# Kernel optimization log

Hardware: AMD Instinct MI355X
Metric: run time of the kernel (lower is better)

Reference implementation:

```python
import jax, jax.numpy as jnp
import numpy as np
import math

B, S, DM, H = 2, 2048, 1024, 16
DH = DM // H  # 64


def setup_inputs() -> dict:
    key = jax.random.key(0)
    ks = jax.random.split(key, 12)
    s = 1.0 / math.sqrt(DM)
    inp = {
        "key": jax.random.normal(ks[0], (B, S, DM), jnp.float32),
        "value": jax.random.normal(ks[1], (B, S, DM), jnp.float32),
        "query": jax.random.normal(ks[2], (B, S, DM), jnp.float32),
        # causal mask: True = masked out (matches masked_fill semantics)
        "mask": jnp.broadcast_to(~jnp.tril(jnp.ones((S, S), bool)), (B, S, S)),
        "Wk": jax.random.normal(ks[3], (DM, DM), jnp.float32) * s,
        "bk": jnp.zeros((DM,), jnp.float32),
        "Wv": jax.random.normal(ks[4], (DM, DM), jnp.float32) * s,
        "bv": jnp.zeros((DM,), jnp.float32),
        "Wq": jax.random.normal(ks[5], (DM, DM), jnp.float32) * s,
        "bq": jnp.zeros((DM,), jnp.float32),
        "Wo": jax.random.normal(ks[6], (DM, DM), jnp.float32) * s,
        "bo": jnp.zeros((DM,), jnp.float32),
    }
    return inp


def _split_heads(x):
    # [B, S, H*DH] -> [B, H, S, DH]
    b, s, _ = x.shape
    return x.reshape(b, s, H, DH).transpose(0, 2, 1, 3)


def reference(key, value, query, mask, Wk, bk, Wv, bv, Wq, bq, Wo, bo):
    key_up = _split_heads(key @ Wk.T + bk)      # [B,H,S,DH]
    value_up = _split_heads(value @ Wv.T + bv)  # [B,H,S,DH]
    query_up = _split_heads(query @ Wq.T + bq) / math.sqrt(DH)
    scores = jnp.einsum("bhqd,bhkd->bhqk", query_up, key_up)  # [B,H,S,S]
    scores = jnp.where(mask[:, None, :, :], jnp.float32(-1e18), scores)
    attn = jax.nn.softmax(scores, axis=-1)
    # dropout is identity in eval mode
    context = jnp.einsum("bhqk,bhkd->bhqd", attn, value_up)
    context = context.transpose(0, 2, 1, 3).reshape(key.shape[0], -1, H * DH)
    output = context @ Wo.T + bo                # [B,S,DM]
    top_attn = attn[:, 0, :, :]                 # [B,S,S]
    return output, top_attn
```

## Files before the change

kernel.cpp:

```cpp
#include <hip/hip_runtime.h>
#include <hip/hip_bf16.h>
#include <math.h>

#define B_ 2
#define S_ 2048
#define DM_ 1024
#define H_ 16
#define DH_ 64

using short8 = __attribute__((ext_vector_type(8))) short;
using f32x4  = __attribute__((ext_vector_type(4))) float;

typedef const __attribute__((address_space(1))) void* gas_cvp;
typedef __attribute__((address_space(3))) void* las_vp;

struct CvtJobs {
    const float* in[7];
    ushort* out[7];
};

__device__ __forceinline__ ushort f2bu(float x) {
    __hip_bfloat16 h = __float2bfloat16(x);
    return *(ushort*)&h;
}

__global__ __launch_bounds__(256) void cvt_bf16(CvtJobs jobs) {
    const int bid = blockIdx.x;
    int j, blk;
    if (bid < 6144) { j = bid >> 11; blk = bid & 2047; }
    else { const int r = bid - 6144; j = 3 + (r >> 9); blk = r & 511; }
    const int idx = (blk * 256 + threadIdx.x) * 8;
    const float* in = jobs.in[j];
    float4 a = *(const float4*)&in[idx];
    float4 b = *(const float4*)&in[idx + 4];
    ushort u[8];
    u[0] = f2bu(a.x); u[1] = f2bu(a.y); u[2] = f2bu(a.z); u[3] = f2bu(a.w);
    u[4] = f2bu(b.x); u[5] = f2bu(b.y); u[6] = f2bu(b.z); u[7] = f2bu(b.w);
    *(int4*)&jobs.out[j][idx] = *(int4*)u;
}

#define GEMM_STAGE(buf, k0v)                                                   \
    {                                                                          \
        _Pragma("unroll")                                                      \
        for (int i = 0; i < 2; i++) {                                          \
            const int s   = i * 256 + tid;                                     \
            const int c   = s >> 7;                                            \
            const int row = s & 127;                                           \
            __builtin_amdgcn_global_load_lds(                                  \
                (gas_cvp)(Ag + (size_t)(i0 + row) * 1024 + (k0v) + c * 8),     \
                (las_vp)&AsB[buf][0][(i * 256 + w * 64) * 8], 16, 0, 0);       \
            __builtin_amdgcn_global_load_lds(                                  \
                (gas_cvp)(Wg + (size_t)(j0 + row) * 1024 + (k0v) + c * 8),     \
                (las_vp)&AsB[buf][1][(i * 256 + w * 64) * 8], 16, 0, 0);       \
        }                                                                      \
    }

#define GEMM_KLOOP()                                                           \
    {                                                                          \
        int bufc = 0;                                                          \
        GEMM_STAGE(0, 0);                                                      \
        GEMM_STAGE(1, 32);                                                     \
        for (int k0 = 0; k0 < 1024; k0 += 32) {                                \
            if (k0 + 32 < 1024)                                                \
                asm volatile("s_waitcnt vmcnt(4)" ::: "memory");               \
            else                                                               \
                asm volatile("s_waitcnt vmcnt(0)" ::: "memory");               \
            __builtin_amdgcn_s_barrier();                                      \
            if (k0 + 64 < 1024) {                                              \
                const int nb = (bufc + 2 >= 3) ? bufc - 1 : bufc + 2;          \
                GEMM_STAGE(nb, k0 + 64);                                       \
            }                                                                  \
            short8 af[4], bf[4];                                               \
            _Pragma("unroll")                                                  \
            for (int m = 0; m < 4; m++)                                        \
                af[m] = *(const short8*)&AsB[bufc][0][((g << 7) + wm * 64 + m * 16 + lr) * 8]; \
            _Pragma("unroll")                                                  \
            for (int n = 0; n < 4; n++)                                        \
                bf[n] = *(const short8*)&AsB[bufc][1][((g << 7) + wn * 64 + n * 16 + lr) * 8]; \
            _Pragma("unroll")                                                  \
            for (int m = 0; m < 4; m++)                                        \
                _Pragma("unroll")                                              \
                for (int n = 0; n < 4; n++)                                    \
                    acc[m][n] = __builtin_amdgcn_mfma_f32_16x16x32_bf16(       \
                        af[m], bf[n], acc[m][n], 0, 0, 0);                     \
            bufc = (bufc + 1 == 3) ? 0 : bufc + 1;                             \
        }                                                                      \
    }

struct ProjJobs {
    const ushort* A[3];
    const ushort* W[3];
    const float* bias[3];
    ushort* C[3];
    float scale[3];
};

__global__ __launch_bounds__(256) void gemm_proj3(ProjJobs jobs)
{
    __shared__ ushort AsB[3][2][4096];

    const int o   = blockIdx.x;
    const int swz = (o & 7) * 96 + (o >> 3);
    const int z   = swz >> 8;
    const int rem = swz & 255;
    const int by  = rem >> 3;
    const int bx  = rem & 7;

    const ushort* Ag = jobs.A[z];
    const ushort* Wg = jobs.W[z];
    const float* bias = jobs.bias[z];
    ushort* C = jobs.C[z];
    const float scale = jobs.scale[z];

    const int tid  = threadIdx.x;
    const int w    = tid >> 6;
    const int lane = tid & 63;
    const int g    = lane >> 4;
    const int lr   = lane & 15;
    const int wm   = w >> 1;
    const int wn   = w & 1;
    const int i0   = by * 128;
    const int j0   = bx * 128;

    f32x4 acc[4][4];
    #pragma unroll
    for (int m = 0; m < 4; m++)
        #pragma unroll
        for (int n = 0; n < 4; n++)
            #pragma unroll
            for (int jj = 0; jj < 4; jj++) acc[m][n][jj] = 0.f;

    GEMM_KLOOP();

    const int colbase = j0 + wn * 64;
    const int rowbase = i0 + wm * 64;
    #pragma unroll
    for (int n = 0; n < 4; n++) {
        const int col = colbase + n * 16 + lr;
        const float bb = bias[col];
        const int hh = col >> 6;
        const int d = col & 63;
        #pragma unroll
        for (int m = 0; m < 4; m++) {
            const int rb = rowbase + m * 16 + g * 4;
            #pragma unroll
            for (int jj = 0; jj < 4; jj++) {
                const float v = (acc[m][n][jj] + bb) * scale;
                const int i = rb + jj;
                const int b = i >> 11;
                const int srow = i & 2047;
                C[(((size_t)b * H_ + hh) * S_ + srow) * DH_ + d] = f2bu(v);
            }
        }
    }
}

__global__ __launch_bounds__(256) void flash_mfma(
    const ushort* __restrict__ Qb, const ushort* __restrict__ Kb,
    const ushort* __restrict__ Vb, __hip_bfloat16* __restrict__ ctx,
    float* __restrict__ m0, float* __restrict__ l0)
{
    const int bid = blockIdx.x;
    const int xcd = bid & 7;
    const int t   = bid >> 3;
    const int P   = (t >> 4) * 8 + xcd;
    const int p   = t & 15;
    const int h   = P & 15;
    const int b   = P >> 4;

    const int qtA = p, qtB = 31 - p;
    const size_t hoff = ((size_t)b * H_ + h) * S_ * DH_;
    const ushort* Qh = Qb + hoff;
    const ushort* Kh = Kb + hoff;
    const ushort* Vh = Vb + hoff;

    __shared__ ushort Ks[64][72];
    __shared__ ushort Vt[64][72];
    __shared__ ushort Ps[4][16][72];

    const int tid  = threadIdx.x;
    const int w    = tid >> 6;
    const int lane = tid & 63;
    const int g    = lane >> 4;
    const int lr   = lane & 15;
    const int q0A  = qtA * 64 + w * 16;
    const int q0B  = qtB * 64 + w * 16;

    short8 qfA0, qfA1, qfB0, qfB1;
    {
        const ushort* qa = Qh + (size_t)(q0A + lr) * DH_ + g * 8;
        qfA0 = *(const short8*)(qa);
        qfA1 = *(const short8*)(qa + 32);
        const ushort* qb = Qh + (size_t)(q0B + lr) * DH_ + g * 8;
        qfB0 = *(const short8*)(qb);
        qfB1 = *(const short8*)(qb + 32);
    }

    f32x4 oA[4], oB[4];
    #pragma unroll
    for (int nc = 0; nc < 4; nc++) {
        oA[nc][0]=0.f; oA[nc][1]=0.f; oA[nc][2]=0.f; oA[nc][3]=0.f;
        oB[nc][0]=0.f; oB[nc][1]=0.f; oB[nc][2]=0.f; oB[nc][3]=0.f;
    }
    float mA = -1e30f, lA = 0.f;
    float mB = -1e30f, lB = 0.f;

    const int nkt = qtB + 1;
    const int c0 = w, c1 = w + 4;

    int4 pk0, pk1, pv0, pv1;
    pk0 = *(const int4*)(Kh + (size_t)lane * DH_ + c0 * 8);
    pk1 = *(const int4*)(Kh + (size_t)lane * DH_ + c1 * 8);
    pv0 = *(const int4*)(Vh + (size_t)lane * DH_ + c0 * 8);
    pv1 = *(const int4*)(Vh + (size_t)lane * DH_ + c1 * 8);

    for (int kt = 0; kt < nkt; kt++) {
        const int kvb = kt * 64;
        __syncthreads();
        {
            *(int4*)&Ks[lane][c0 * 8] = pk0;
            *(int4*)&Ks[lane][c1 * 8] = pk1;
            ushort vv[8];
            *(int4*)vv = pv0;
            #pragma unroll
            for (int j2 = 0; j2 < 8; j2++) Vt[c0 * 8 + j2][lane] = vv[j2];
            *(int4*)vv = pv1;
            #pragma unroll
            for (int j2 = 0; j2 < 8; j2++) Vt[c1 * 8 + j2][lane] = vv[j2];
        }
        if (kt + 1 < nkt) {
            const size_t roff = (size_t)(kvb + 64 + lane) * DH_;
            pk0 = *(const int4*)(Kh + roff + c0 * 8);
            pk1 = *(const int4*)(Kh + roff + c1 * 8);
            pv0 = *(const int4*)(Vh + roff + c0 * 8);
            pv1 = *(const int4*)(Vh + roff + c1 * 8);
        }
        __syncthreads();

        #pragma unroll
        for (int u = 0; u < 2; u++) {
            if (u == 0 && kt > qtA) continue;
            const int qt_u  = (u == 0) ? qtA : qtB;
            const int q0w   = (u == 0) ? q0A : q0B;
            const short8 qf0 = (u == 0) ? qfA0 : qfB0;
            const short8 qf1 = (u == 0) ? qfA1 : qfB1;
            float& m_r = (u == 0) ? mA : mB;
            float& l_r = (u == 0) ? lA : lB;
            f32x4* o   = (u == 0) ? oA : oB;
            const int qglob = q0w + lr;

            f32x4 st[4];
            #pragma unroll
            for (int mt = 0; mt < 4; mt++) { st[mt][0]=0.f; st[mt][1]=0.f; st[mt][2]=0.f; st[mt][3]=0.f; }
            __builtin_amdgcn_s_setprio(1);
            #pragma unroll
            for (int mt = 0; mt < 4; mt++) {
                short8 ka = *(const short8*)&Ks[16 * mt + lr][8 * g];
                short8 kb = *(const short8*)&Ks[16 * mt + lr][32 + 8 * g];
                st[mt] = __builtin_amdgcn_mfma_f32_16x16x32_bf16(ka, qf0, st[mt], 0, 0, 0);
                st[mt] = __builtin_amdgcn_mfma_f32_16x16x32_bf16(kb, qf1, st[mt], 0, 0, 0);
            }
            __builtin_amdgcn_s_setprio(0);

            if (kt == qt_u) {
                #pragma unroll
                for (int mt = 0; mt < 4; mt++)
                    #pragma unroll
                    for (int jj = 0; jj < 4; jj++)
                        if (kvb + 16 * mt + 4 * g + jj > qglob) st[mt][jj] = -1e30f;
            }

            float pmax = st[0][0];
            #pragma unroll
            for (int mt = 0; mt < 4; mt++)
                #pragma unroll
                for (int jj = 0; jj < 4; jj++)
                    pmax = fmaxf(pmax, st[mt][jj]);
            pmax = fmaxf(pmax, __shfl_xor(pmax, 16));
            pmax = fmaxf(pmax, __shfl_xor(pmax, 32));

            const bool defer = __all(pmax - m_r <= 8.0f);
            float mnew = m_r, scv = 1.0f;
            if (!defer) {
                mnew = fmaxf(m_r, pmax);
                scv  = __expf(m_r - mnew);
            }

            float lsum = 0.f;
            #pragma unroll
            for (int mt = 0; mt < 4; mt++)
                #pragma unroll
                for (int jj = 0; jj < 4; jj++) {
                    st[mt][jj] = __expf(st[mt][jj] - mnew);
                    lsum += st[mt][jj];
                }
            lsum += __shfl_xor(lsum, 16);
            lsum += __shfl_xor(lsum, 32);
            l_r = l_r * scv + lsum;
            m_r = mnew;

            if (!defer) {
                float sc0 = __shfl(scv, 4 * g + 0);
                float sc1 = __shfl(scv, 4 * g + 1);
                float sc2 = __shfl(scv, 4 * g + 2);
                float sc3 = __shfl(scv, 4 * g + 3);
                #pragma unroll
                for (int nc = 0; nc < 4; nc++) {
                    o[nc][0] *= sc0; o[nc][1] *= sc1;
                    o[nc][2] *= sc2; o[nc][3] *= sc3;
                }
            }

            #pragma unroll
            for (int mt = 0; mt < 4; mt++) {
                ushort u4[4];
                #pragma unroll
                for (int jj = 0; jj < 4; jj++) u4[jj] = f2bu(st[mt][jj]);
                *(uint2*)&Ps[w][lr][16 * mt + 4 * g] = *(uint2*)u4;
            }

            short8 pa0 = *(const short8*)&Ps[w][lr][8 * g];
            short8 pa1 = *(const short8*)&Ps[w][lr][32 + 8 * g];
            __builtin_amdgcn_s_setprio(1);
            #pragma unroll
            for (int nc = 0; nc < 4; nc++) {
                short8 v0 = *(const short8*)&Vt[16 * nc + lr][8 * g];
                short8 v1 = *(const short8*)&Vt[16 * nc + lr][32 + 8 * g];
                o[nc] = __builtin_amdgcn_mfma_f32_16x16x32_bf16(pa0, v0, o[nc], 0, 0, 0);
                o[nc] = __builtin_amdgcn_mfma_f32_16x16x32_bf16(pa1, v1, o[nc], 0, 0, 0);
            }
            __builtin_amdgcn_s_setprio(0);
        }
    }

    #pragma unroll
    for (int u = 0; u < 2; u++) {
        const int q0w = (u == 0) ? q0A : q0B;
        const float m_r = (u == 0) ? mA : mB;
        const float l_r = (u == 0) ? lA : lB;
        const f32x4* o  = (u == 0) ? oA : oB;
        const float linv = 1.0f / l_r;
        float li0 = __shfl(linv, 4 * g + 0);
        float li1 = __shfl(linv, 4 * g + 1);
        float li2 = __shfl(linv, 4 * g + 2);
        float li3 = __shfl(linv, 4 * g + 3);
        #pragma unroll
        for (int reg = 0; reg < 4; reg++) {
            const int qrow = q0w + 4 * g + reg;
            const float li = (reg == 0) ? li0 : (reg == 1) ? li1 : (reg == 2) ? li2 : li3;
            __hip_bfloat16* cp = ctx + ((size_t)b * S_ + qrow) * DM_ + h * DH_;
            #pragma unroll
            for (int nc = 0; nc < 4; nc++)
                cp[16 * nc + lr] = __float2bfloat16(o[nc][reg] * li);
        }
        if (h == 0 && lane < 16) {
            m0[b * S_ + q0w + lane] = m_r;
            l0[b * S_ + q0w + lane] = l_r;
        }
    }
}

__global__ __launch_bounds__(256) void tail_fused(
    const ushort* __restrict__ ctxb, const ushort* __restrict__ Wg_,
    const float* __restrict__ bo, float* __restrict__ out,
    const ushort* __restrict__ Qb, const ushort* __restrict__ Kb,
    const float* __restrict__ m0, const float* __restrict__ l0,
    float* __restrict__ attn)
{
    __shared__ ushort AsB[3][2][4096];
    const int o = blockIdx.x;
    const int tid = threadIdx.x;
    const int w    = tid >> 6;
    const int lane = tid & 63;
    const int g    = lane >> 4;
    const int lr   = lane & 15;

    if (o < 256) {
        const int swz = (o & 7) * 32 + (o >> 3);
        const int by  = swz >> 3;
        const int bx  = swz & 7;
        const int wm  = w >> 1;
        const int wn  = w & 1;
        const int i0  = by * 128;
        const int j0  = bx * 128;
        const ushort* Ag = ctxb;
        const ushort* Wg = Wg_;

        f32x4 acc[4][4];
        #pragma unroll
        for (int m = 0; m < 4; m++)
            #pragma unroll
            for (int n = 0; n < 4; n++)
                #pragma unroll
                for (int jj = 0; jj < 4; jj++) acc[m][n][jj] = 0.f;

        GEMM_KLOOP();

        const int colbase = j0 + wn * 64;
        const int rowbase = i0 + wm * 64;
        #pragma unroll
        for (int n = 0; n < 4; n++) {
            const int col = colbase + n * 16 + lr;
            const float bb = bo[col];
            #pragma unroll
            for (int m = 0; m < 4; m++) {
                const int rb = rowbase + m * 16 + g * 4;
                #pragma unroll
                for (int jj = 0; jj < 4; jj++)
                    out[(size_t)(rb + jj) * DM_ + col] = acc[m][n][jj] + bb;
            }
        }
        return;
    }

    const int t   = o - 256;
    const int kt  = t & 31;
    const int qt2 = (t >> 5) & 31;
    const int b   = t >> 10;
    float* ap = attn + (size_t)b * S_ * S_;

    if (kt > qt2) {
        const int row = qt2 * 64 + (tid >> 2);
        const int col = kt * 64 + (tid & 3) * 16;
        float4 z = {0.f, 0.f, 0.f, 0.f};
        float* rp = ap + (size_t)row * S_ + col;
        *(float4*)&rp[0]  = z;
        *(float4*)&rp[4]  = z;
        *(float4*)&rp[8]  = z;
        *(float4*)&rp[12] = z;
        return;
    }

    ushort (*Ks)[72] = (ushort(*)[72])&AsB[0][0][0];
    const int q0w = qt2 * 64 + w * 16;
    const int kvb = kt * 64;
    const size_t hoff = (size_t)b * H_ * S_ * DH_;
    const ushort* Qh = Qb + hoff;
    const ushort* Kh = Kb + hoff;

    #pragma unroll
    for (int i = 0; i < 2; i++) {
        const int c = w + 4 * i;
        int4 k4 = *(const int4*)(Kh + (size_t)(kvb + lane) * DH_ + c * 8);
        *(int4*)&Ks[lane][c * 8] = k4;
    }

    short8 qf0, qf1;
    {
        const ushort* qp = Qh + (size_t)(q0w + lr) * DH_ + g * 8;
        qf0 = *(const short8*)(qp);
        qf1 = *(const short8*)(qp + 32);
    }
    const int qglob = q0w + lr;
    const float mv   = m0[b * S_ + qglob];
    const float linv = 1.0f / l0[b * S_ + qglob];
    __syncthreads();

    f32x4 st[4];
    #pragma unroll
    for (int mt = 0; mt < 4; mt++) { st[mt][0]=0.f; st[mt][1]=0.f; st[mt][2]=0.f; st[mt][3]=0.f; }
    #pragma unroll
    for (int mt = 0; mt < 4; mt++) {
        short8 ka = *(const short8*)&Ks[16 * mt + lr][8 * g];
        short8 kb = *(const short8*)&Ks[16 * mt + lr][32 + 8 * g];
        st[mt] = __builtin_amdgcn_mfma_f32_16x16x32_bf16(ka, qf0, st[mt], 0, 0, 0);
        st[mt] = __builtin_amdgcn_mfma_f32_16x16x32_bf16(kb, qf1, st[mt], 0, 0, 0);
    }

    float* rowp = ap + (size_t)qglob * S_ + kvb;
    #pragma unroll
    for (int mt = 0; mt < 4; mt++) {
        float4 ov;
        float v[4];
        #pragma unroll
        for (int jj = 0; jj < 4; jj++) {
            const int kv = 16 * mt + 4 * g + jj;
            float pv = __expf(st[mt][jj] - mv) * linv;
            v[jj] = (kvb + kv > qglob) ? 0.f : pv;
        }
        ov.x = v[0]; ov.y = v[1]; ov.z = v[2]; ov.w = v[3];
        *(float4*)&rowp[16 * mt + 4 * g] = ov;
    }
}

extern "C" void kernel_launch(void* const* d_in, const int* in_sizes, int n_in,
                              void* d_out, int out_size, void* d_ws, size_t ws_size,
                              hipStream_t stream)
{
    const float* key   = (const float*)d_in[0];
    const float* value = (const float*)d_in[1];
    const float* query = (const float*)d_in[2];
    const float* Wk = (const float*)d_in[4];
    const float* bk = (const float*)d_in[5];
    const float* Wv = (const float*)d_in[6];
    const float* bv = (const float*)d_in[7];
    const float* Wq = (const float*)d_in[8];
    const float* bq = (const float*)d_in[9];
    const float* Wo = (const float*)d_in[10];
    const float* bo = (const float*)d_in[11];

    char* ws = (char*)d_ws;
    const size_t per = (size_t)B_ * H_ * S_ * DH_;
    const size_t wsz = (size_t)DM_ * DM_;
    __hip_bfloat16* Qp   = (__hip_bfloat16*)ws;
    __hip_bfloat16* Kp   = Qp + per;
    __hip_bfloat16* Vp   = Kp + per;
    __hip_bfloat16* ctxb = Vp + per;
    __hip_bfloat16* qc   = ctxb + per;
    __hip_bfloat16* kc   = qc + per;
    __hip_bfloat16* vc   = kc + per;
    __hip_bfloat16* wqb  = vc + per;
    __hip_bfloat16* wkb  = wqb + wsz;
    __hip_bfloat16* wvb  = wkb + wsz;
    __hip_bfloat16* wob  = wvb + wsz;
    float* m0 = (float*)(wob + wsz);
    float* l0 = m0 + B_ * S_;

    float* out   = (float*)d_out;
    float* topat = out + (size_t)B_ * S_ * DM_;

    CvtJobs jobs;
    jobs.in[0] = query; jobs.out[0] = (ushort*)qc;
    jobs.in[1] = key;   jobs.out[1] = (ushort*)kc;
    jobs.in[2] = value; jobs.out[2] = (ushort*)vc;
    jobs.in[3] = Wq;    jobs.out[3] = (ushort*)wqb;
    jobs.in[4] = Wk;    jobs.out[4] = (ushort*)wkb;
    jobs.in[5] = Wv;    jobs.out[5] = (ushort*)wvb;
    jobs.in[6] = Wo;    jobs.out[6] = (ushort*)wob;
    cvt_bf16<<<6144 + 4 * 512, 256, 0, stream>>>(jobs);

    ProjJobs pj;
    pj.A[0] = (const ushort*)qc; pj.W[0] = (const ushort*)wqb; pj.bias[0] = bq;
    pj.C[0] = (ushort*)Qp; pj.scale[0] = 0.125f;
    pj.A[1] = (const ushort*)kc; pj.W[1] = (const ushort*)wkb; pj.bias[1] = bk;
    pj.C[1] = (ushort*)Kp; pj.scale[1] = 1.0f;
    pj.A[2] = (const ushort*)vc; pj.W[2] = (const ushort*)wvb; pj.bias[2] = bv;
    pj.C[2] = (ushort*)Vp; pj.scale[2] = 1.0f;
    gemm_proj3<<<768, 256, 0, stream>>>(pj);

    flash_mfma<<<512, 256, 0, stream>>>(
        (const ushort*)Qp, (const ushort*)Kp, (const ushort*)Vp, ctxb, m0, l0);

    tail_fused<<<256 + B_ * 32 * 32, 256, 0, stream>>>(
        (const ushort*)ctxb, (const ushort*)wob, bo, out,
        (const ushort*)Qp, (const ushort*)Kp, m0, l0, topat);
}
```

Measured before the change: 154.0 us.

## Enlarge projection GEMM tiles to 256x256 with 512 threads and 4-stage pipeline

Rewrites the fused QKV projection GEMM to use 256x256 output tiles per workgroup of 8 waves, each computing 128x64, with a 4-buffer LDS ring prefetched three stages ahead and MFMA priority raised. The grid drops from 768 to 192 blocks. The goal is more reuse of the A and W tiles per LDS load and better latency hiding. The costs are 128KB of LDS per block, higher register pressure from 32 accumulators, and fewer blocks than CUs (192 vs 256), which leaves some CUs idle.

```diff
diff --git a/kernel.cpp b/kernel.cpp
--- a/kernel.cpp
+++ b/kernel.cpp
@@ -37,6 +37,120 @@
     u[0] = f2bu(a.x); u[1] = f2bu(a.y); u[2] = f2bu(a.z); u[3] = f2bu(a.w);
     u[4] = f2bu(b.x); u[5] = f2bu(b.y); u[6] = f2bu(b.z); u[7] = f2bu(b.w);
     *(int4*)&jobs.out[j][idx] = *(int4*)u;
+}
+
+struct ProjJobs {
+    const ushort* A[3];
+    const ushort* W[3];
+    const float* bias[3];
+    ushort* C[3];
+    float scale[3];
+};
+
+#define PSTAGE(buf, k0v)                                                       \
+    {                                                                          \
+        _Pragma("unroll")                                                      \
+        for (int i = 0; i < 2; i++) {                                          \
+            const int s   = i * 512 + tid;                                     \
+            const int c   = s >> 8;                                            \
+            const int row = s & 255;                                           \
+            __builtin_amdgcn_global_load_lds(                                  \
+                (gas_cvp)(Ag + (size_t)(i0 + row) * 1024 + (k0v) + c * 8),     \
+                (las_vp)&SH[(buf) * 16384 + (i * 512 + w * 64) * 8], 16, 0, 0);\
+            __builtin_amdgcn_global_load_lds(                                  \
+                (gas_cvp)(Wg + (size_t)(j0 + row) * 1024 + (k0v) + c * 8),     \
+                (las_vp)&SH[(buf) * 16384 + 8192 + (i * 512 + w * 64) * 8],    \
+                16, 0, 0);                                                     \
+        }                                                                      \
+    }
+
+__global__ __launch_bounds__(512) void gemm_proj3(ProjJobs jobs)
+{
+    __shared__ ushort SH[65536];
+
+    const int o   = blockIdx.x;
+    const int swz = (o & 7) * 24 + (o >> 3);
+    const int z   = swz >> 6;
+    const int rem = swz & 63;
+    const int by  = rem >> 2;
+    const int bx  = rem & 3;
+
+    const ushort* Ag = jobs.A[z];
+    const ushort* Wg = jobs.W[z];
+    const float* bias = jobs.bias[z];
+    ushort* C = jobs.C[z];
+    const float scale = jobs.scale[z];
+
+    const int tid  = threadIdx.x;
+    const int w    = tid >> 6;
+    const int lane = tid & 63;
+    const int g    = lane >> 4;
+    const int lr   = lane & 15;
+    const int wm   = w >> 2;
+    const int wn   = w & 3;
+    const int i0   = by * 256;
+    const int j0   = bx * 256;
+
+    f32x4 acc[8][4];
+    #pragma unroll
+    for (int m = 0; m < 8; m++)
+        #pragma unroll
+        for (int n = 0; n < 4; n++)
+            #pragma unroll
+            for (int jj = 0; jj < 4; jj++) acc[m][n][jj] = 0.f;
+
+    PSTAGE(0, 0);
+    PSTAGE(1, 32);
+    PSTAGE(2, 64);
+
+    for (int kt = 0; kt < 32; kt++) {
+        if (kt < 30)       asm volatile("s_waitcnt vmcnt(8)" ::: "memory");
+        else if (kt == 30) asm volatile("s_waitcnt vmcnt(4)" ::: "memory");
+        else               asm volatile("s_waitcnt vmcnt(0)" ::: "memory");
+        __builtin_amdgcn_s_barrier();
+
+        if (kt + 3 < 32) PSTAGE((kt + 3) & 3, (kt + 3) * 32);
+
+        const int ab = (kt & 3) * 16384;
+        short8 af[8], bf[4];
+        #pragma unroll
+        for (int m = 0; m < 8; m++)
+            af[m] = *(const short8*)&SH[ab + (g * 256 + wm * 128 + m * 16 + lr) * 8];
+        #pragma unroll
+        for (int n = 0; n < 4; n++)
+            bf[n] = *(const short8*)&SH[ab + 8192 + (g * 256 + wn * 64 + n * 16 + lr) * 8];
+
+        __builtin_amdgcn_s_setprio(1);
+        #pragma unroll
+        for (int m = 0; m < 8; m++)
+            #pragma unroll
+            for (int n = 0; n < 4; n++)
+                acc[m][n] = __builtin_amdgcn_mfma_f32_16x16x32_bf16(
+                    af[m], bf[n], acc[m][n], 0, 0, 0);
+        __builtin_amdgcn_s_setprio(0);
+    }
+
+    const int colbase = j0 + wn * 64;
+    const int rowbase = i0 + wm * 128;
+    #pragma unroll
+    for (int n = 0; n < 4; n++) {
+        const int col = colbase + n * 16 + lr;
+        const float bb = bias[col];
+        const int hh = col >> 6;
+        const int d = col & 63;
+        #pragma unroll
+        for (int m = 0; m < 8; m++) {
+            const int rb = rowbase + m * 16 + g * 4;
+            #pragma unroll
+            for (int jj = 0; jj < 4; jj++) {
+                const float v = (acc[m][n][jj] + bb) * scale;
+                const int i = rb + jj;
+                const int b = i >> 11;
+                const int srow = i & 2047;
+                C[(((size_t)b * H_ + hh) * S_ + srow) * DH_ + d] = f2bu(v);
+            }
+        }
+    }
 }
 
 #define GEMM_STAGE(buf, k0v)                                                   \
@@ -87,74 +201,6 @@
         }                                                                      \
     }
 
-struct ProjJobs {
-    const ushort* A[3];
-    const ushort* W[3];
-    const float* bias[3];
-    ushort* C[3];
-    float scale[3];
-};
-
-__global__ __launch_bounds__(256) void gemm_proj3(ProjJobs jobs)
-{
-    __shared__ ushort AsB[3][2][4096];
-
-    const int o   = blockIdx.x;
-    const int swz = (o & 7) * 96 + (o >> 3);
-    const int z   = swz >> 8;
-    const int rem = swz & 255;
-    const int by  = rem >> 3;
-    const int bx  = rem & 7;
-
-    const ushort* Ag = jobs.A[z];
-    const ushort* Wg = jobs.W[z];
-    const float* bias = jobs.bias[z];
-    ushort* C = jobs.C[z];
-    const float scale = jobs.scale[z];
-
-    const int tid  = threadIdx.x;
-    const int w    = tid >> 6;
-    const int lane = tid & 63;
-    const int g    = lane >> 4;
-    const int lr   = lane & 15;
-    const int wm   = w >> 1;
-    const int wn   = w & 1;
-    const int i0   = by * 128;
-    const int j0   = bx * 128;
-
-    f32x4 acc[4][4];
-    #pragma unroll
-    for (int m = 0; m < 4; m++)
-        #pragma unroll
-        for (int n = 0; n < 4; n++)
-            #pragma unroll
-            for (int jj = 0; jj < 4; jj++) acc[m][n][jj] = 0.f;
-
-    GEMM_KLOOP();
-
-    const int colbase = j0 + wn * 64;
-    const int rowbase = i0 + wm * 64;
-    #pragma unroll
-    for (int n = 0; n < 4; n++) {
-        const int col = colbase + n * 16 + lr;
-        const float bb = bias[col];
-        const int hh = col >> 6;
-        const int d = col & 63;
-        #pragma unroll
-        for (int m = 0; m < 4; m++) {
-            const int rb = rowbase + m * 16 + g * 4;
-            #pragma unroll
-            for (int jj = 0; jj < 4; jj++) {
-                const float v = (acc[m][n][jj] + bb) * scale;
-                const int i = rb + jj;
-                const int b = i >> 11;
-                const int srow = i & 2047;
-                C[(((size_t)b * H_ + hh) * S_ + srow) * DH_ + d] = f2bu(v);
-            }
-        }
-    }
-}
-
 __global__ __launch_bounds__(256) void flash_mfma(
     const ushort* __restrict__ Qb, const ushort* __restrict__ Kb,
     const ushort* __restrict__ Vb, __hip_bfloat16* __restrict__ ctx,
@@ -536,7 +582,7 @@
     pj.C[1] = (ushort*)Kp; pj.scale[1] = 1.0f;
     pj.A[2] = (const ushort*)vc; pj.W[2] = (const ushort*)wvb; pj.bias[2] = bv;
     pj.C[2] = (ushort*)Vp; pj.scale[2] = 1.0f;
-    gemm_proj3<<<768, 256, 0, stream>>>(pj);
+    gemm_proj3<<<192, 512, 0, stream>>>(pj);
 
     flash_mfma<<<512, 256, 0, stream>>>(
         (const ushort*)Qp, (const ushort*)Kp, (const ushort*)Vp, ctxb, m0, l0);
```

New measurement: 154.6 us. No clear change (+0.4%).

## Widen flash attention blocks to 8 waves covering 128-row query tiles

Applied to the files above, without the earlier changes.

The flash attention kernel now launches 256 blocks of 512 threads instead of 512 blocks of 256. Each block handles two 128-row query tiles, paired for causal balance, with each wave owning 16 rows. The causal diagonal is now computed per wave. Each K/V tile staged in shared memory is reused by twice as many query rows, which halves K/V global traffic and staging per query. The cost is fewer blocks on the device, larger barrier groups, and waves whose diagonal comes earlier sitting idle while others finish.

```diff
diff --git a/kernel.cpp b/kernel.cpp
--- a/kernel.cpp
+++ b/kernel.cpp
@@ -155,7 +155,7 @@
     }
 }
 
-__global__ __launch_bounds__(256) void flash_mfma(
+__global__ __launch_bounds__(512) void flash_mfma(
     const ushort* __restrict__ Qb, const ushort* __restrict__ Kb,
     const ushort* __restrict__ Vb, __hip_bfloat16* __restrict__ ctx,
     float* __restrict__ m0, float* __restrict__ l0)
@@ -163,12 +163,11 @@
     const int bid = blockIdx.x;
     const int xcd = bid & 7;
     const int t   = bid >> 3;
-    const int P   = (t >> 4) * 8 + xcd;
-    const int p   = t & 15;
+    const int P   = (t >> 3) * 8 + xcd;
+    const int p   = t & 7;
     const int h   = P & 15;
     const int b   = P >> 4;
 
-    const int qtA = p, qtB = 31 - p;
     const size_t hoff = ((size_t)b * H_ + h) * S_ * DH_;
     const ushort* Qh = Qb + hoff;
     const ushort* Kh = Kb + hoff;
@@ -176,15 +175,18 @@
 
     __shared__ ushort Ks[64][72];
     __shared__ ushort Vt[64][72];
-    __shared__ ushort Ps[4][16][72];
+    __shared__ ushort Ps[8][16][72];
 
     const int tid  = threadIdx.x;
     const int w    = tid >> 6;
     const int lane = tid & 63;
     const int g    = lane >> 4;
     const int lr   = lane & 15;
-    const int q0A  = qtA * 64 + w * 16;
-    const int q0B  = qtB * 64 + w * 16;
+    const int q0A  = p * 128 + w * 16;
+    const int q0B  = (15 - p) * 128 + w * 16;
+    const int diagA = (q0A + 15) >> 6;
+    const int diagB = (q0B + 15) >> 6;
+    const int nkt   = 2 * (16 - p);
 
     short8 qfA0, qfA1, qfB0, qfB1;
     {
@@ -205,42 +207,30 @@
     float mA = -1e30f, lA = 0.f;
     float mB = -1e30f, lB = 0.f;
 
-    const int nkt = qtB + 1;
-    const int c0 = w, c1 = w + 4;
-
-    int4 pk0, pk1, pv0, pv1;
-    pk0 = *(const int4*)(Kh + (size_t)lane * DH_ + c0 * 8);
-    pk1 = *(const int4*)(Kh + (size_t)lane * DH_ + c1 * 8);
-    pv0 = *(const int4*)(Vh + (size_t)lane * DH_ + c0 * 8);
-    pv1 = *(const int4*)(Vh + (size_t)lane * DH_ + c1 * 8);
+    int4 pk = *(const int4*)(Kh + (size_t)lane * DH_ + w * 8);
+    int4 pv = *(const int4*)(Vh + (size_t)lane * DH_ + w * 8);
 
     for (int kt = 0; kt < nkt; kt++) {
         const int kvb = kt * 64;
         __syncthreads();
         {
-            *(int4*)&Ks[lane][c0 * 8] = pk0;
-            *(int4*)&Ks[lane][c1 * 8] = pk1;
+            *(int4*)&Ks[lane][w * 8] = pk;
             ushort vv[8];
-            *(int4*)vv = pv0;
-            #pragma unroll
-            for (int j2 = 0; j2 < 8; j2++) Vt[c0 * 8 + j2][lane] = vv[j2];
-            *(int4*)vv = pv1;
-            #pragma unroll
-            for (int j2 = 0; j2 < 8; j2++) Vt[c1 * 8 + j2][lane] = vv[j2];
+            *(int4*)vv = pv;
+            #pragma unroll
+            for (int j2 = 0; j2 < 8; j2++) Vt[w * 8 + j2][lane] = vv[j2];
         }
         if (kt + 1 < nkt) {
-            const size_t roff = (size_t)(kvb + 64 + lane) * DH_;
-            pk0 = *(const int4*)(Kh + roff + c0 * 8);
-            pk1 = *(const int4*)(Kh + roff + c1 * 8);
-            pv0 = *(const int4*)(Vh + roff + c0 * 8);
-            pv1 = *(const int4*)(Vh + roff + c1 * 8);
+            const size_t roff = (size_t)(kvb + 64 + lane) * DH_ + w * 8;
+            pk = *(const int4*)(Kh + roff);
+            pv = *(const int4*)(Vh + roff);
         }
         __syncthreads();
 
         #pragma unroll
         for (int u = 0; u < 2; u++) {
-            if (u == 0 && kt > qtA) continue;
-            const int qt_u  = (u == 0) ? qtA : qtB;
+            const int diag = (u == 0) ? diagA : diagB;
+            if (kt > diag) continue;
             const int q0w   = (u == 0) ? q0A : q0B;
             const short8 qf0 = (u == 0) ? qfA0 : qfB0;
             const short8 qf1 = (u == 0) ? qfA1 : qfB1;
@@ -262,7 +252,7 @@
             }
             __builtin_amdgcn_s_setprio(0);
 
-            if (kt == qt_u) {
+            if (kt == diag) {
                 #pragma unroll
                 for (int mt = 0; mt < 4; mt++)
                     #pragma unroll
@@ -538,7 +528,7 @@
     pj.C[2] = (ushort*)Vp; pj.scale[2] = 1.0f;
     gemm_proj3<<<768, 256, 0, stream>>>(pj);
 
-    flash_mfma<<<512, 256, 0, stream>>>(
+    flash_mfma<<<256, 512, 0, stream>>>(
         (const ushort*)Qp, (const ushort*)Kp, (const ushort*)Vp, ctxb, m0, l0);
 
     tail_fused<<<256 + B_ * 32 * 32, 256, 0, stream>>>(
```

Measured after the change: 150.1 us. 1.03x faster.
